# Kernel optimization log

Measured on AMD Instinct MI355X. Metric: run time of the kernel, lower is better.

The kernel has to match this reference:

```python
import jax, jax.numpy as jnp
import numpy as np

SIGMA = 1.0


def setup_inputs() -> dict:
    key = jax.random.key(0)
    z = jax.random.normal(key, (8192, 128), dtype=jnp.float32)
    return {"z": z}


def reference(z) -> jnp.ndarray:
    # Pairwise squared L2 distance via the GEMM identity:
    #   ||zi - zj||^2 = ||zi||^2 + ||zj||^2 - 2 zi . zj
    # Same math as broadcast-subtract-square-sum, without the [N,N,D] intermediate.
    sq = jnp.sum(z * z, axis=-1)                      # [N]
    gram = z @ z.T                                    # [N, N]
    d2 = sq[:, None] + sq[None, :] - 2.0 * gram       # [N, N]
    d2 = jnp.maximum(d2, 0.0)  # clamp tiny negatives from cancellation
    return jnp.exp(-d2 / SIGMA)
```

## Files before the change

### kernel.cpp

```cpp
#include <hip/hip_runtime.h>
#include <hip/hip_bf16.h>

#define N 8192
#define Dd 128

typedef short short8 __attribute__((ext_vector_type(8)));
typedef float floatx4 __attribute__((ext_vector_type(4)));

static __device__ inline unsigned short f2bf(float f) {
    unsigned int u = __float_as_uint(f);
    return (unsigned short)((u + 0x7fffu + ((u >> 16) & 1u)) >> 16);
}
static __device__ inline float bf2f(unsigned short b) {
    return __uint_as_float(((unsigned int)b) << 16);
}

__global__ __launch_bounds__(256) void prep_kernel(const float* __restrict__ z,
                                                   unsigned short* __restrict__ zb,
                                                   float* __restrict__ sq) {
    int row  = blockIdx.x * 4 + (threadIdx.x >> 6);
    int lane = threadIdx.x & 63;
    float2 v = ((const float2*)z)[row * 64 + lane];
    unsigned short b0 = f2bf(v.x);
    unsigned short b1 = f2bf(v.y);
    float f0 = bf2f(b0), f1 = bf2f(b1);
    ushort2 st; st.x = b0; st.y = b1;
    ((ushort2*)zb)[row * 64 + lane] = st;
    float s = f0 * f0 + f1 * f1;
    #pragma unroll
    for (int off = 32; off > 0; off >>= 1) s += __shfl_down(s, off, 64);
    if (lane == 0) sq[row] = s;
}

__global__ __launch_bounds__(256, 4) void pairsim_kernel(const unsigned short* __restrict__ zb,
                                                         const float* __restrict__ sq,
                                                         float* __restrict__ out) {
    __shared__ unsigned short lA[64 * 128];
    __shared__ unsigned short lB[64 * 128];

    int bx = blockIdx.x, by = blockIdx.y;
    int colBase = bx * 64, rowBase = by * 64;
    int t  = threadIdx.x;
    int r0 = t >> 4, cg = t & 15;

    const uint4* gA = (const uint4*)(zb + (size_t)rowBase * Dd);
    const uint4* gB = (const uint4*)(zb + (size_t)colBase * Dd);
    uint4 va[4], vb[4];
    #pragma unroll
    for (int i = 0; i < 4; i++) va[i] = gA[(r0 + i * 16) * 16 + cg];
    #pragma unroll
    for (int i = 0; i < 4; i++) vb[i] = gB[(r0 + i * 16) * 16 + cg];

    int scg = ((cg ^ r0) * 8);
    #pragma unroll
    for (int i = 0; i < 4; i++) *(uint4*)&lA[(r0 + i * 16) * 128 + scg] = va[i];
    #pragma unroll
    for (int i = 0; i < 4; i++) *(uint4*)&lB[(r0 + i * 16) * 128 + scg] = vb[i];
    __syncthreads();

    int w = t >> 6, lane = t & 63;
    int wr = (w >> 1) * 32, wc = (w & 1) * 32;
    int m = lane & 15, quad = lane >> 4;

    floatx4 zero = {0.f, 0.f, 0.f, 0.f};
    floatx4 acc[2][2];
    #pragma unroll
    for (int i = 0; i < 2; i++)
        #pragma unroll
        for (int j = 0; j < 2; j++) acc[i][j] = zero;

    #pragma unroll
    for (int ks = 0; ks < 4; ks++) {
        short8 af[2], bfr[2];
        int c = ks * 4 + quad;
        #pragma unroll
        for (int i = 0; i < 2; i++)
            af[i] = *(const short8*)&lA[(wr + i * 16 + m) * 128 + ((c ^ m) * 8)];
        #pragma unroll
        for (int j = 0; j < 2; j++)
            bfr[j] = *(const short8*)&lB[(wc + j * 16 + m) * 128 + ((c ^ m) * 8)];
        #pragma unroll
        for (int i = 0; i < 2; i++)
            #pragma unroll
            for (int j = 0; j < 2; j++)
                acc[i][j] = __builtin_amdgcn_mfma_f32_16x16x32_bf16(af[i], bfr[j], acc[i][j], 0, 0, 0);
    }

    #pragma unroll
    for (int i = 0; i < 2; i++) {
        #pragma unroll
        for (int r = 0; r < 4; r++) {
            int row = rowBase + wr + i * 16 + quad * 4 + r;
            float sr = sq[row];
            #pragma unroll
            for (int j = 0; j < 2; j++) {
                int col = colBase + wc + j * 16 + m;
                float sc = sq[col];
                float g = acc[i][j][r];
                float e = fminf(2.0f * g - sr - sc, 0.0f);
                out[(size_t)row * N + col] = __expf(e);
            }
        }
    }
}

extern "C" void kernel_launch(void* const* d_in, const int* in_sizes, int n_in,
                              void* d_out, int out_size, void* d_ws, size_t ws_size,
                              hipStream_t stream) {
    const float* z = (const float*)d_in[0];
    unsigned short* zb = (unsigned short*)d_ws;
    float* sqv = (float*)((char*)d_ws + (size_t)N * Dd * sizeof(unsigned short));
    float* out = (float*)d_out;

    prep_kernel<<<N / 4, 256, 0, stream>>>(z, zb, sqv);
    pairsim_kernel<<<dim3(128, 128), 256, 0, stream>>>(zb, sqv, out);
}
```

Measured before the change: 260.1 us.

## Replace LDS-tiled blocks with per-wave strips streaming B tiles from global

Each wave now owns a 16-row strip and walks 64 column tiles of 16 across a 1024-column segment. The A fragments stay in registers and the B fragments are register double-buffered straight from global memory, so the kernel no longer uses LDS, __syncthreads, or the 16K-block grid. This cuts launch and block setup cost and reuses the A fragments across many tiles. In exchange, each wave re-reads B from L2 per 16x16 tile and stores only 16 consecutive floats per row per iteration, which may hurt store coalescing on an output-write-bound kernel.

```diff
diff --git a/kernel.cpp b/kernel.cpp
--- a/kernel.cpp
+++ b/kernel.cpp
@@ -32,74 +32,51 @@
     if (lane == 0) sq[row] = s;
 }
 
-__global__ __launch_bounds__(256, 4) void pairsim_kernel(const unsigned short* __restrict__ zb,
-                                                         const float* __restrict__ sq,
-                                                         float* __restrict__ out) {
-    __shared__ unsigned short lA[64 * 128];
-    __shared__ unsigned short lB[64 * 128];
-
-    int bx = blockIdx.x, by = blockIdx.y;
-    int colBase = bx * 64, rowBase = by * 64;
-    int t  = threadIdx.x;
-    int r0 = t >> 4, cg = t & 15;
-
-    const uint4* gA = (const uint4*)(zb + (size_t)rowBase * Dd);
-    const uint4* gB = (const uint4*)(zb + (size_t)colBase * Dd);
-    uint4 va[4], vb[4];
-    #pragma unroll
-    for (int i = 0; i < 4; i++) va[i] = gA[(r0 + i * 16) * 16 + cg];
-    #pragma unroll
-    for (int i = 0; i < 4; i++) vb[i] = gB[(r0 + i * 16) * 16 + cg];
-
-    int scg = ((cg ^ r0) * 8);
-    #pragma unroll
-    for (int i = 0; i < 4; i++) *(uint4*)&lA[(r0 + i * 16) * 128 + scg] = va[i];
-    #pragma unroll
-    for (int i = 0; i < 4; i++) *(uint4*)&lB[(r0 + i * 16) * 128 + scg] = vb[i];
-    __syncthreads();
-
-    int w = t >> 6, lane = t & 63;
-    int wr = (w >> 1) * 32, wc = (w & 1) * 32;
+__global__ __launch_bounds__(256) void pairsim_kernel(const unsigned short* __restrict__ zb,
+                                                      const float* __restrict__ sq,
+                                                      float* __restrict__ out) {
+    int wid  = blockIdx.x * 4 + (threadIdx.x >> 6);
+    int lane = threadIdx.x & 63;
     int m = lane & 15, quad = lane >> 4;
 
-    floatx4 zero = {0.f, 0.f, 0.f, 0.f};
-    floatx4 acc[2][2];
+    int rowBase = (wid >> 3) * 16;
+    int colSeg  = (wid & 7) * 1024;
+
+    const short8* Ab = (const short8*)(zb + (size_t)rowBase * Dd);
+    short8 af[4];
     #pragma unroll
-    for (int i = 0; i < 2; i++)
+    for (int ks = 0; ks < 4; ks++) af[ks] = Ab[m * 16 + ks * 4 + quad];
+
+    float4 srv = *(const float4*)&sq[rowBase + quad * 4];
+
+    const short8* Bb = (const short8*)(zb + (size_t)colSeg * Dd);
+    short8 bn[4];
+    #pragma unroll
+    for (int ks = 0; ks < 4; ks++) bn[ks] = Bb[m * 16 + ks * 4 + quad];
+    float scn = sq[colSeg + m];
+
+    for (int ct = 0; ct < 64; ct++) {
+        short8 bf[4];
         #pragma unroll
-        for (int j = 0; j < 2; j++) acc[i][j] = zero;
+        for (int ks = 0; ks < 4; ks++) bf[ks] = bn[ks];
+        float sc = scn;
 
-    #pragma unroll
-    for (int ks = 0; ks < 4; ks++) {
-        short8 af[2], bfr[2];
-        int c = ks * 4 + quad;
+        int ctn = (ct + 1) & 63;
+        const short8* Bn = (const short8*)(zb + (size_t)(colSeg + ctn * 16) * Dd);
         #pragma unroll
-        for (int i = 0; i < 2; i++)
-            af[i] = *(const short8*)&lA[(wr + i * 16 + m) * 128 + ((c ^ m) * 8)];
+        for (int ks = 0; ks < 4; ks++) bn[ks] = Bn[m * 16 + ks * 4 + quad];
+        scn = sq[colSeg + ctn * 16 + m];
+
+        floatx4 acc = {0.f, 0.f, 0.f, 0.f};
         #pragma unroll
-        for (int j = 0; j < 2; j++)
-            bfr[j] = *(const short8*)&lB[(wc + j * 16 + m) * 128 + ((c ^ m) * 8)];
-        #pragma unroll
-        for (int i = 0; i < 2; i++)
-            #pragma unroll
-            for (int j = 0; j < 2; j++)
-                acc[i][j] = __builtin_amdgcn_mfma_f32_16x16x32_bf16(af[i], bfr[j], acc[i][j], 0, 0, 0);
-    }
+        for (int ks = 0; ks < 4; ks++)
+            acc = __builtin_amdgcn_mfma_f32_16x16x32_bf16(af[ks], bf[ks], acc, 0, 0, 0);
 
-    #pragma unroll
-    for (int i = 0; i < 2; i++) {
+        int col = colSeg + ct * 16 + m;
         #pragma unroll
         for (int r = 0; r < 4; r++) {
-            int row = rowBase + wr + i * 16 + quad * 4 + r;
-            float sr = sq[row];
-            #pragma unroll
-            for (int j = 0; j < 2; j++) {
-                int col = colBase + wc + j * 16 + m;
-                float sc = sq[col];
-                float g = acc[i][j][r];
-                float e = fminf(2.0f * g - sr - sc, 0.0f);
-                out[(size_t)row * N + col] = __expf(e);
-            }
+            float e = fminf(2.0f * acc[r] - srv[r] - sc, 0.0f);
+            out[(size_t)(rowBase + quad * 4 + r) * N + col] = __expf(e);
         }
     }
 }
@@ -113,5 +90,5 @@
     float* out = (float*)d_out;
 
     prep_kernel<<<N / 4, 256, 0, stream>>>(z, zb, sqv);
-    pairsim_kernel<<<dim3(128, 128), 256, 0, stream>>>(zb, sqv, out);
+    pairsim_kernel<<<1024, 256, 0, stream>>>(zb, sqv, out);
 }
```

Result: slower. 355.6 us (+36.8%).
